# Kernel tuning notes

Measured on AMD Instinct MI355X. Metric: run time of the kernel, lower is better.

## Reference

```python
import jax, jax.numpy as jnp
import numpy as np

N = 80000      # points (voxels)
M = 2048       # windows
C = 128        # d_model
H = 8          # heads
D = C // H     # head_dim = 16
B = 2          # batch size
HB, WB = 32, 32  # BEV window grid shape


def setup_inputs() -> dict:
    key = jax.random.key(0)
    k1, k2, k3, k4 = jax.random.split(key, 4)
    x = jax.random.normal(k1, (N, C), dtype=jnp.float32)
    Wqkv = jax.random.normal(k2, (3 * C, C), dtype=jnp.float32) * 0.05
    Wproj = jax.random.normal(k3, (C, C), dtype=jnp.float32) * 0.05
    bproj = jax.random.normal(k4, (C,), dtype=jnp.float32) * 0.05
    # ragged windows: near-equal contiguous split of N into M groups
    base = N // M
    rem = N - base * M
    counts_np = base + (np.arange(M) < rem).astype(np.int64)
    offsets_np = np.concatenate([[0], np.cumsum(counts_np)[:-1]]).astype(np.int64)
    batch_win_inds_np = np.repeat(np.arange(M, dtype=np.int64), counts_np)
    wid = np.arange(M, dtype=np.int64)
    coords_np = np.stack([wid // (HB * WB), (wid % (HB * WB)) // WB, wid % WB], axis=1)
    return {
        "x": x, "Wqkv": Wqkv, "Wproj": Wproj, "bproj": bproj,
        "offsets": jnp.asarray(offsets_np), "counts": jnp.asarray(counts_np),
        "batch_win_inds": jnp.asarray(batch_win_inds_np),
        "batch_win_coords": jnp.asarray(coords_np),
    }


def _pool3x3(feat, coords):
    # sparse 3x3 sum-pool (stride 1, pad 1) over BEV grid, via dense scatter + shifted sums
    F_ = feat.shape[-1]
    grid = jnp.zeros((B, HB, WB, F_), feat.dtype).at[coords[:, 0], coords[:, 1], coords[:, 2]].set(feat)
    p = jnp.pad(grid, ((0, 0), (1, 1), (1, 1), (0, 0)))
    pooled = sum(p[:, dy:dy + HB, dx:dx + WB] for dy in range(3) for dx in range(3))
    return pooled[coords[:, 0], coords[:, 1], coords[:, 2]]


def reference(x, Wqkv, Wproj, bproj, offsets, counts, batch_win_inds, batch_win_coords):
    n = x.shape[0]
    qkv = (x @ Wqkv.T).reshape(n, 3, H, D)
    q = jax.nn.relu(qkv[:, 0])  # [N, H, D]
    k = jax.nn.relu(qkv[:, 1])
    v = qkv[:, 2]
    # per-window cumulative K^T V (scatter_matmul_kv): [M, H, D, D]
    kv_pt = jnp.einsum('nhd,nhe->nhde', k, v)
    kv = jax.ops.segment_sum(kv_pt, batch_win_inds, num_segments=M)
    # per-window key sum: [M, H, D]
    s = jax.ops.segment_sum(k, batch_win_inds, num_segments=M)
    # 3x3 sum pool over neighboring windows
    kv = _pool3x3(kv.reshape(M, H * D * D), batch_win_coords).reshape(M, H, D, D)
    s = _pool3x3(s.reshape(M, H * D), batch_win_coords).reshape(M, H, D)
    # Q @ C readout (scatter_matmul_qc)
    y = jnp.einsum('nhd,nhde->nhe', q, kv[batch_win_inds])
    z = jnp.sum(s[batch_win_inds] * q, axis=-1, keepdims=True)
    y = y / (z + 1e-6)
    y = y.reshape(n, C)
    return y @ Wproj.T + bproj
```

## Files before the change

### kernel.cpp

```cpp
#include <hip/hip_runtime.h>

#define MWIN 2048
#define HH 8

typedef _Float16 half8 __attribute__((ext_vector_type(8)));
typedef _Float16 half4 __attribute__((ext_vector_type(4)));
typedef float f32x4 __attribute__((ext_vector_type(4)));

__device__ __forceinline__ int win_swz(int bid) {
    return (bid & 7) * 256 + (bid >> 3);
}

__global__ __launch_bounds__(256) void k_prep_w(const float* __restrict__ Wqkv,
                                                const float* __restrict__ Wproj,
                                                _Float16* __restrict__ fq,
                                                _Float16* __restrict__ fp) {
    int tid = blockIdx.x * 256 + threadIdx.x;
    const float* src;
    _Float16* dst;
    if (tid < 6144) { src = Wqkv; dst = fq; }
    else {
        tid -= 6144;
        if (tid >= 2048) return;
        src = Wproj; dst = fp;
    }
    int lane = tid & 63, r = tid >> 6;
    int ct = r & 3, ks = (r >> 2) & 3, cg = r >> 4;
    int m = lane & 15, q = lane >> 4;
    const float* s_ = src + (size_t)(cg * 64 + ct * 16 + m) * 128 + q * 8 + ks * 32;
    float4 f0 = *(const float4*)s_;
    float4 f1 = *(const float4*)(s_ + 4);
    half8 h;
    h[0] = (_Float16)f0.x; h[1] = (_Float16)f0.y; h[2] = (_Float16)f0.z; h[3] = (_Float16)f0.w;
    h[4] = (_Float16)f1.x; h[5] = (_Float16)f1.y; h[6] = (_Float16)f1.z; h[7] = (_Float16)f1.w;
    *(half8*)(dst + (size_t)tid * 8) = h;
}

__global__ __launch_bounds__(512) void k_qkv_win(const float* __restrict__ x,
                                                 const half8* __restrict__ fq,
                                                 const int* __restrict__ offsets,
                                                 const int* __restrict__ counts,
                                                 _Float16* __restrict__ q_h,
                                                 float* __restrict__ kv_t,
                                                 float* __restrict__ s) {
    __shared__ _Float16 xs[48][136];
    __shared__ _Float16 qk[48][392];
    int w = win_swz(blockIdx.x);
    int off = offsets[w], cnt = counts[w];
    int tid = threadIdx.x;

    #pragma unroll
    for (int it = 0; it < 3; ++it) {
        int j = it * 512 + tid;
        int row = j >> 5, c4 = j & 31;
        int sr = row < cnt ? row : cnt - 1;
        float4 f = *(const float4*)(x + (size_t)(off + sr) * 128 + c4 * 4);
        half4 hv;
        hv[0] = (_Float16)f.x; hv[1] = (_Float16)f.y;
        hv[2] = (_Float16)f.z; hv[3] = (_Float16)f.w;
        *(half4*)&xs[row][c4 * 4] = hv;
    }
    __syncthreads();

    int h = tid >> 6, lane = tid & 63;
    int m = lane & 15, q = lane >> 4;

    half8 a[3][4];
    #pragma unroll
    for (int rt = 0; rt < 3; ++rt)
        #pragma unroll
        for (int ks = 0; ks < 4; ++ks)
            a[rt][ks] = *(const half8*)&xs[rt * 16 + m][q * 8 + ks * 32];

    #pragma unroll
    for (int j = 0; j < 3; ++j) {
        int ctg = h * 3 + j;
        int cg = ctg >> 2, ctl = ctg & 3;
        half8 bfr[4];
        #pragma unroll
        for (int ks = 0; ks < 4; ++ks)
            bfr[ks] = fq[((size_t)cg * 16 + ks * 4 + ctl) * 64 + lane];
        bool dorelu = ctg < 16;
        #pragma unroll
        for (int rt = 0; rt < 3; ++rt) {
            f32x4 acc = {};
            #pragma unroll
            for (int ks = 0; ks < 4; ++ks)
                acc = __builtin_amdgcn_mfma_f32_16x16x32_f16(a[rt][ks], bfr[ks], acc, 0, 0, 0);
            #pragma unroll
            for (int reg = 0; reg < 4; ++reg) {
                float vv = acc[reg];
                if (dorelu) vv = fmaxf(vv, 0.f);
                qk[rt * 16 + q * 4 + reg][ctg * 16 + m] = (_Float16)vv;
            }
        }
    }
    __syncthreads();

    #pragma unroll
    for (int it = 0; it < 2; ++it) {
        int idx = it * 512 + tid;
        int row = idx >> 4, c8 = idx & 15;
        if (row < cnt)
            *(half8*)(q_h + (size_t)(off + row) * 128 + c8 * 8) = *(const half8*)&qk[row][c8 * 8];
    }

    int d = lane & 15, eq = lane >> 4;
    float a0 = 0.f, a1 = 0.f, a2 = 0.f, a3 = 0.f, sa = 0.f;
    for (int p = 0; p < cnt; ++p) {
        float kk = (float)qk[p][128 + h * 16 + d];
        half4 v4 = *(const half4*)&qk[p][256 + h * 16 + eq * 4];
        a0 += kk * (float)v4[0];
        a1 += kk * (float)v4[1];
        a2 += kk * (float)v4[2];
        a3 += kk * (float)v4[3];
        sa += kk;
    }
    float* o = kv_t + (((size_t)(w * HH + h)) << 8);
    o[(eq * 4 + 0) * 16 + d] = a0;
    o[(eq * 4 + 1) * 16 + d] = a1;
    o[(eq * 4 + 2) * 16 + d] = a2;
    o[(eq * 4 + 3) * 16 + d] = a3;
    if (eq == 0) s[(((size_t)(w * HH + h)) << 4) + d] = sa;
}

__global__ __launch_bounds__(512) void k_attn_proj(const _Float16* __restrict__ q_h,
                                                   const float* __restrict__ kv_t,
                                                   const float* __restrict__ s,
                                                   const half8* __restrict__ fp,
                                                   const float* __restrict__ bproj,
                                                   const int* __restrict__ offsets,
                                                   const int* __restrict__ counts,
                                                   float* __restrict__ out) {
    __shared__ _Float16 y_t[48][136];
    __shared__ float o_t[48][132];
    int w = win_swz(blockIdx.x);
    int h = threadIdx.x >> 6;
    int lane = threadIdx.x & 63;
    int col = lane & 15;
    int kq = lane >> 4;
    int off = offsets[w], cnt = counts[w];
    bool klive = kq < 2;
    int koff = (kq & 1) * 8;

    int b = w >> 10, yy = (w >> 5) & 31, xx = w & 31;
    f32x4 k0 = {}, k1 = {}, s0 = {}, s1 = {};
    if (klive) {
        #pragma unroll
        for (int dy = -1; dy <= 1; ++dy)
            #pragma unroll
            for (int dx = -1; dx <= 1; ++dx) {
                int ny = yy + dy, nx = xx + dx;
                if (ny < 0 || ny >= 32 || nx < 0 || nx >= 32) continue;
                int nw = (b << 10) | (ny << 5) | nx;
                const float* kb = kv_t + (((size_t)(nw * HH + h)) << 8) + col * 16 + koff;
                k0 += *(const f32x4*)kb;
                k1 += *(const f32x4*)(kb + 4);
                const float* sb = s + (((size_t)(nw * HH + h)) << 4) + koff;
                s0 += *(const f32x4*)sb;
                s1 += *(const f32x4*)(sb + 4);
            }
    }
    half8 a_kv, a_s;
    #pragma unroll
    for (int i = 0; i < 4; ++i) {
        a_kv[i] = (_Float16)k0[i]; a_kv[4 + i] = (_Float16)k1[i];
        a_s[i]  = (_Float16)s0[i]; a_s[4 + i]  = (_Float16)s1[i];
    }

    #pragma unroll
    for (int c = 0; c < 3; ++c) {
        int p = c * 16 + col;
        int pc = p < cnt ? p : cnt - 1;
        half8 b_q = *(const half8*)(q_h + (size_t)(off + pc) * 128 + h * 16 + koff);
        f32x4 acc = {};
        acc = __builtin_amdgcn_mfma_f32_16x16x32_f16(a_kv, b_q, acc, 0, 0, 0);
        f32x4 accs = {};
        accs = __builtin_amdgcn_mfma_f32_16x16x32_f16(a_s, b_q, accs, 0, 0, 0);
        float zinv = 1.f / (accs[0] + 1e-6f);
        half4 yo;
        #pragma unroll
        for (int i = 0; i < 4; ++i) yo[i] = (_Float16)(acc[i] * zinv);
        *(half4*)&y_t[p][h * 16 + kq * 4] = yo;
    }
    __syncthreads();

    int m = col, q = kq;
    int ct = h;
    int cg = ct >> 2, ctl = ct & 3;
    half8 bfr[4];
    #pragma unroll
    for (int ks = 0; ks < 4; ++ks)
        bfr[ks] = fp[((size_t)cg * 16 + ks * 4 + ctl) * 64 + lane];
    float bv = bproj[ct * 16 + m];
    #pragma unroll
    for (int rt = 0; rt < 3; ++rt) {
        f32x4 acc = (f32x4){bv, bv, bv, bv};
        #pragma unroll
        for (int ks = 0; ks < 4; ++ks) {
            half8 af = *(const half8*)&y_t[rt * 16 + m][q * 8 + ks * 32];
            acc = __builtin_amdgcn_mfma_f32_16x16x32_f16(af, bfr[ks], acc, 0, 0, 0);
        }
        #pragma unroll
        for (int reg = 0; reg < 4; ++reg)
            o_t[rt * 16 + q * 4 + reg][ct * 16 + m] = acc[reg];
    }
    __syncthreads();

    #pragma unroll
    for (int it = 0; it < 3; ++it) {
        int j = it * 512 + threadIdx.x;
        int r = j >> 5, c4 = j & 31;
        if (r < cnt)
            *(float4*)(out + ((size_t)(off + r) << 7) + c4 * 4) = *(const float4*)&o_t[r][c4 * 4];
    }
}

extern "C" void kernel_launch(void* const* d_in, const int* in_sizes, int n_in,
                              void* d_out, int out_size, void* d_ws, size_t ws_size,
                              hipStream_t stream) {
    const float* x     = (const float*)d_in[0];
    const float* Wqkv  = (const float*)d_in[1];
    const float* Wproj = (const float*)d_in[2];
    const float* bproj = (const float*)d_in[3];
    const int*   offsets = (const int*)d_in[4];
    const int*   counts  = (const int*)d_in[5];

    int N = in_sizes[0] / 128;

    char* ws = (char*)d_ws;
    float* kv_t = (float*)ws;                                    ws += (size_t)MWIN * HH * 256 * 4;
    float* s    = (float*)ws;                                    ws += (size_t)MWIN * HH * 16 * 4;
    _Float16* q_h    = (_Float16*)ws;                            ws += (size_t)N * 128 * 2;
    _Float16* fq     = (_Float16*)ws;                            ws += (size_t)6144 * 8 * 2;
    _Float16* fp     = (_Float16*)ws;                            ws += (size_t)2048 * 8 * 2;
    float* out  = (float*)d_out;

    k_prep_w<<<32, 256, 0, stream>>>(Wqkv, Wproj, fq, fp);

    k_qkv_win<<<MWIN, 512, 0, stream>>>(x, (const half8*)fq, offsets, counts,
                                        q_h, kv_t, s);

    k_attn_proj<<<MWIN, 512, 0, stream>>>(q_h, kv_t, s, (const half8*)fp, bproj,
                                          offsets, counts, out);
}
```

Before: 153.4 us.

## Compute per-window K^T V and key sums with MFMA via transposed LDS tiles

Replaces the scalar per-lane loop over window points that accumulated K^T V and key sums with MFMA instructions. K and V are written transposed into LDS tiles (padded to 64 points, with padding zeroed) so they can serve directly as MFMA operands, and the key sum is computed as an MFMA against a ones vector. The x staging buffer is reused for the K/V tiles to keep LDS usage in check, which adds an extra barrier. The scalar loop was serial in the point count, and this removes it at the cost of some zero-padding work and the layout change.

After: 150.3 us. 1.02x faster.

```diff
diff --git a/kernel.cpp b/kernel.cpp
--- a/kernel.cpp
+++ b/kernel.cpp
@@ -43,8 +43,11 @@
                                                  _Float16* __restrict__ q_h,
                                                  float* __restrict__ kv_t,
                                                  float* __restrict__ s) {
-    __shared__ _Float16 xs[48][136];
-    __shared__ _Float16 qk[48][392];
+    __shared__ __attribute__((aligned(16))) _Float16 ubuf[18432];
+    __shared__ __attribute__((aligned(16))) _Float16 q_lds[48][136];
+    _Float16 (*kT)[16][72] = (_Float16(*)[16][72])ubuf;
+    _Float16 (*vT)[16][72] = (_Float16(*)[16][72])(ubuf + 9216);
+
     int w = win_swz(blockIdx.x);
     int off = offsets[w], cnt = counts[w];
     int tid = threadIdx.x;
@@ -58,7 +61,7 @@
         half4 hv;
         hv[0] = (_Float16)f.x; hv[1] = (_Float16)f.y;
         hv[2] = (_Float16)f.z; hv[3] = (_Float16)f.w;
-        *(half4*)&xs[row][c4 * 4] = hv;
+        *(half4*)&ubuf[row * 136 + c4 * 4] = hv;
     }
     __syncthreads();
 
@@ -70,7 +73,14 @@
     for (int rt = 0; rt < 3; ++rt)
         #pragma unroll
         for (int ks = 0; ks < 4; ++ks)
-            a[rt][ks] = *(const half8*)&xs[rt * 16 + m][q * 8 + ks * 32];
+            a[rt][ks] = *(const half8*)&ubuf[(rt * 16 + m) * 136 + q * 8 + ks * 32];
+    __syncthreads();
+
+    {
+        int zh = tid >> 6, zd = (tid >> 2) & 15, zp = 48 + (tid & 3) * 4;
+        *(half4*)&kT[zh][zd][zp] = (half4){};
+        *(half4*)&vT[zh][zd][zp] = (half4){};
+    }
 
     #pragma unroll
     for (int j = 0; j < 3; ++j) {
@@ -80,18 +90,30 @@
         #pragma unroll
         for (int ks = 0; ks < 4; ++ks)
             bfr[ks] = fq[((size_t)cg * 16 + ks * 4 + ctl) * 64 + lane];
-        bool dorelu = ctg < 16;
         #pragma unroll
         for (int rt = 0; rt < 3; ++rt) {
             f32x4 acc = {};
             #pragma unroll
             for (int ks = 0; ks < 4; ++ks)
                 acc = __builtin_amdgcn_mfma_f32_16x16x32_f16(a[rt][ks], bfr[ks], acc, 0, 0, 0);
-            #pragma unroll
-            for (int reg = 0; reg < 4; ++reg) {
-                float vv = acc[reg];
-                if (dorelu) vv = fmaxf(vv, 0.f);
-                qk[rt * 16 + q * 4 + reg][ctg * 16 + m] = (_Float16)vv;
+            int p0 = rt * 16 + q * 4;
+            if (ctg < 8) {
+                #pragma unroll
+                for (int reg = 0; reg < 4; ++reg)
+                    q_lds[p0 + reg][ctg * 16 + m] = (_Float16)fmaxf(acc[reg], 0.f);
+            } else if (ctg < 16) {
+                int head = ctg - 8;
+                half4 hv;
+                #pragma unroll
+                for (int reg = 0; reg < 4; ++reg)
+                    hv[reg] = (_Float16)((p0 + reg < cnt) ? fmaxf(acc[reg], 0.f) : 0.f);
+                *(half4*)&kT[head][m][p0] = hv;
+            } else {
+                int head = ctg - 16;
+                half4 hv;
+                #pragma unroll
+                for (int reg = 0; reg < 4; ++reg) hv[reg] = (_Float16)acc[reg];
+                *(half4*)&vT[head][m][p0] = hv;
             }
         }
     }
@@ -102,26 +124,25 @@
         int idx = it * 512 + tid;
         int row = idx >> 4, c8 = idx & 15;
         if (row < cnt)
-            *(half8*)(q_h + (size_t)(off + row) * 128 + c8 * 8) = *(const half8*)&qk[row][c8 * 8];
-    }
-
-    int d = lane & 15, eq = lane >> 4;
-    float a0 = 0.f, a1 = 0.f, a2 = 0.f, a3 = 0.f, sa = 0.f;
-    for (int p = 0; p < cnt; ++p) {
-        float kk = (float)qk[p][128 + h * 16 + d];
-        half4 v4 = *(const half4*)&qk[p][256 + h * 16 + eq * 4];
-        a0 += kk * (float)v4[0];
-        a1 += kk * (float)v4[1];
-        a2 += kk * (float)v4[2];
-        a3 += kk * (float)v4[3];
-        sa += kk;
-    }
-    float* o = kv_t + (((size_t)(w * HH + h)) << 8);
-    o[(eq * 4 + 0) * 16 + d] = a0;
-    o[(eq * 4 + 1) * 16 + d] = a1;
-    o[(eq * 4 + 2) * 16 + d] = a2;
-    o[(eq * 4 + 3) * 16 + d] = a3;
-    if (eq == 0) s[(((size_t)(w * HH + h)) << 4) + d] = sa;
+            *(half8*)(q_h + (size_t)(off + row) * 128 + c8 * 8) = *(const half8*)&q_lds[row][c8 * 8];
+    }
+
+    half8 a1 = *(const half8*)&kT[h][m][q * 8];
+    half8 a2 = *(const half8*)&kT[h][m][32 + q * 8];
+    half8 b1 = *(const half8*)&vT[h][m][q * 8];
+    half8 b2 = *(const half8*)&vT[h][m][32 + q * 8];
+    half8 ones;
+    #pragma unroll
+    for (int i = 0; i < 8; ++i) ones[i] = (_Float16)1.0f;
+    f32x4 kva = {};
+    kva = __builtin_amdgcn_mfma_f32_16x16x32_f16(a1, b1, kva, 0, 0, 0);
+    kva = __builtin_amdgcn_mfma_f32_16x16x32_f16(a2, b2, kva, 0, 0, 0);
+    f32x4 sa4 = {};
+    sa4 = __builtin_amdgcn_mfma_f32_16x16x32_f16(a1, ones, sa4, 0, 0, 0);
+    sa4 = __builtin_amdgcn_mfma_f32_16x16x32_f16(a2, ones, sa4, 0, 0, 0);
+    *(f32x4*)(kv_t + (((size_t)(w * HH + h)) << 8) + m * 16 + q * 4) = kva;
+    if (m == 0)
+        *(f32x4*)(s + (((size_t)(w * HH + h)) << 4) + q * 4) = sa4;
 }
 
 __global__ __launch_bounds__(512) void k_attn_proj(const _Float16* __restrict__ q_h,
```
